# Optimization experiments

Hardware: AMD Instinct MI355X
Metric: run time of the kernel (lower is better)

The kernel has to match this reference:

```python
import jax, jax.numpy as jnp
import numpy as np

N_HEADS = 4
N_GROUPS = 32
EPS = 1e-5


def setup_inputs() -> dict:
    key = jax.random.key(0)
    ks = jax.random.split(key, 6)
    c = 512
    x = jax.random.normal(ks[0], (4, c, 64, 64), dtype=jnp.float32)
    # conv1x1 weights ~ kaiming-ish scale
    s = 1.0 / np.sqrt(c)
    wq = jax.random.normal(ks[1], (c, c), dtype=jnp.float32) * s
    wk = jax.random.normal(ks[2], (c, c), dtype=jnp.float32) * s
    wv = jax.random.normal(ks[3], (c, c), dtype=jnp.float32) * s
    wp = jax.random.normal(ks[4], (c, c), dtype=jnp.float32) * s
    zeros = jnp.zeros((c,), dtype=jnp.float32)
    return {
        "x": x,
        "gn_w": jnp.ones((c,), dtype=jnp.float32), "gn_b": zeros,
        "wq": wq, "bq": zeros, "wk": wk, "bk": zeros,
        "wv": wv, "bv": zeros, "wp": wp, "bp": zeros,
    }


def _group_norm(x, w, b):
    bsz, c, h, wd = x.shape
    xg = x.reshape(bsz, N_GROUPS, c // N_GROUPS, h, wd)
    mean = xg.mean(axis=(2, 3, 4), keepdims=True)
    var = xg.var(axis=(2, 3, 4), keepdims=True)
    xg = (xg - mean) * jax.lax.rsqrt(var + EPS)
    x = xg.reshape(bsz, c, h, wd)
    return x * w[None, :, None, None] + b[None, :, None, None]


def _conv1x1(x, w, b):
    # x: (b,c,h,w), w: (out,in) -> (b,out,h,w)
    return jnp.einsum('bchw,oc->bohw', x, w) + b[None, :, None, None]


def reference(x, gn_w, gn_b, wq, bq, wk, bk, wv, bv, wp, bp):
    bsz, c, h, wd = x.shape
    hd = c // N_HEADS
    hw = h * wd
    x_n = _group_norm(x, gn_w, gn_b)
    q = _conv1x1(x_n, wq, bq)
    k = _conv1x1(x_n, wk, bk)
    v = _conv1x1(x_n, wv, bv)

    def to_heads(t):
        # (b,c,h,w) -> (b, n_heads, hw, head_dim)
        return t.reshape(bsz, N_HEADS, hd, hw).transpose(0, 1, 3, 2)

    q, k, v = to_heads(q), to_heads(k), to_heads(v)
    scale = hd ** (-0.5)
    attn = jnp.einsum('bhqd,bhkd->bhqk', q, k) * scale  # (b,H,hw,hw)
    attn = jax.nn.softmax(attn, axis=-1)
    out = jnp.einsum('bhqk,bhkd->bhqd', attn, v)
    out = out.transpose(0, 1, 3, 2).reshape(bsz, c, h, wd)
    out = _conv1x1(out, wp, bp)
    return x + out
```

## Files before the change

### kernel.cpp

```cpp
#include <hip/hip_runtime.h>
#include <math.h>

typedef __attribute__((ext_vector_type(8))) short short8;
typedef __attribute__((ext_vector_type(4))) float floatx4;
typedef __attribute__((ext_vector_type(8))) unsigned short ushort8v;
typedef __attribute__((ext_vector_type(4))) unsigned short ushort4v;

#define HW 4096
#define CCH 512
#define NB 4
#define NH 4
#define HD 128

__device__ __forceinline__ unsigned short f2bf(float f) {
    union { float f; unsigned int u; } c; c.f = f;
    unsigned int u = c.u;
    u += 0x7FFFu + ((u >> 16) & 1u);
    return (unsigned short)(u >> 16);
}

__global__ void conv_w(const float* __restrict__ w0, const float* __restrict__ w1,
                       const float* __restrict__ w2, const float* __restrict__ w3,
                       unsigned short* __restrict__ dst) {
    const float* src = blockIdx.y == 0 ? w0 : blockIdx.y == 1 ? w1 : blockIdx.y == 2 ? w2 : w3;
    unsigned short* d = dst + (size_t)blockIdx.y * 262144;
    int i = blockIdx.x * 256 + threadIdx.x;
    float4 v = ((const float4*)src)[i];
    ushort4v o;
    o[0] = f2bf(v.x); o[1] = f2bf(v.y); o[2] = f2bf(v.z); o[3] = f2bf(v.w);
    ((ushort4v*)d)[i] = o;
}

__global__ void gn_stats(const float* __restrict__ x, float* __restrict__ stats) {
    int bg = blockIdx.x;
    int b = bg >> 5, g = bg & 31;
    const float4* p = (const float4*)(x + ((size_t)b * CCH + g * 16) * HW);
    float s = 0.f, ss = 0.f;
    for (int i = threadIdx.x; i < 16384; i += 256) {
        float4 v = p[i];
        s  += v.x + v.y + v.z + v.w;
        ss += v.x * v.x + v.y * v.y + v.z * v.z + v.w * v.w;
    }
    #pragma unroll
    for (int off = 32; off > 0; off >>= 1) {
        s  += __shfl_down(s, off, 64);
        ss += __shfl_down(ss, off, 64);
    }
    __shared__ float sm[4], sm2[4];
    int wid = threadIdx.x >> 6;
    if ((threadIdx.x & 63) == 0) { sm[wid] = s; sm2[wid] = ss; }
    __syncthreads();
    if (threadIdx.x == 0) {
        float ts = sm[0] + sm[1] + sm[2] + sm[3];
        float tss = sm2[0] + sm2[1] + sm2[2] + sm2[3];
        float mean = ts * (1.f / 65536.f);
        float var = tss * (1.f / 65536.f) - mean * mean;
        stats[bg * 2] = mean;
        stats[bg * 2 + 1] = rsqrtf(var + 1e-5f);
    }
}

__global__ void gn_apply(const float* __restrict__ x, const float* __restrict__ gnw,
                         const float* __restrict__ gnb, const float* __restrict__ stats,
                         unsigned short* __restrict__ xt) {
    int s = blockIdx.x * 256 + threadIdx.x;
    int g = blockIdx.y, b = blockIdx.z;
    float mean = stats[(b * 32 + g) * 2];
    float rstd = stats[(b * 32 + g) * 2 + 1];
    const float* xb = x + ((size_t)b * CCH + g * 16) * HW + s;
    unsigned short outv[16];
    #pragma unroll
    for (int cl = 0; cl < 16; cl++) {
        int c = g * 16 + cl;
        float v = xb[(size_t)cl * HW];
        v = (v - mean) * rstd * gnw[c] + gnb[c];
        outv[cl] = f2bf(v);
    }
    unsigned short* dst = xt + ((size_t)b * HW + s) * CCH + g * 16;
    *(ushort8v*)dst       = *(ushort8v*)&outv[0];
    *(ushort8v*)(dst + 8) = *(ushort8v*)&outv[8];
}

#define LDP 72
template <int MODE>
__global__ __launch_bounds__(256, 2) void gemm_nt(
    const unsigned short* __restrict__ A, long long aStride,
    const unsigned short* __restrict__ Bm, long long bStride,
    const float* __restrict__ bias, float scale,
    const float* __restrict__ resid, long long rStride,
    void* __restrict__ Cp, long long cStride, int ldc) {
    __shared__ unsigned short lA[128 * LDP];
    __shared__ unsigned short lB[128 * LDP];
    const int tid = threadIdx.x;
    const int lane = tid & 63;
    const int wid = tid >> 6;
    const int z = blockIdx.z;
    const unsigned short* Ab = A + (size_t)z * aStride + (size_t)blockIdx.x * 128 * 512;
    const unsigned short* Bb = Bm + (size_t)z * bStride + (size_t)blockIdx.y * 128 * 512;

    floatx4 acc[4][4];
    #pragma unroll
    for (int i = 0; i < 4; i++)
        #pragma unroll
        for (int j = 0; j < 4; j++) acc[i][j] = (floatx4)0.f;

    const int wm = (wid >> 1) * 64;
    const int wn = (wid & 1) * 64;
    const int l15 = lane & 15;
    const int l4 = lane >> 4;

    for (int k0 = 0; k0 < 512; k0 += 64) {
        #pragma unroll
        for (int i = 0; i < 4; i++) {
            int idx = i * 256 + tid;
            int row = idx >> 3;
            int kc = (idx & 7) * 8;
            *(ushort8v*)&lA[row * LDP + kc] = *(const ushort8v*)&Ab[(size_t)row * 512 + k0 + kc];
            *(ushort8v*)&lB[row * LDP + kc] = *(const ushort8v*)&Bb[(size_t)row * 512 + k0 + kc];
        }
        __syncthreads();
        #pragma unroll
        for (int kk = 0; kk < 2; kk++) {
            short8 af[4], bf[4];
            #pragma unroll
            for (int i = 0; i < 4; i++)
                af[i] = *(const short8*)&lA[(wm + i * 16 + l15) * LDP + kk * 32 + l4 * 8];
            #pragma unroll
            for (int j = 0; j < 4; j++)
                bf[j] = *(const short8*)&lB[(wn + j * 16 + l15) * LDP + kk * 32 + l4 * 8];
            #pragma unroll
            for (int i = 0; i < 4; i++)
                #pragma unroll
                for (int j = 0; j < 4; j++)
                    acc[i][j] = __builtin_amdgcn_mfma_f32_16x16x32_bf16(af[i], bf[j], acc[i][j], 0, 0, 0);
        }
        __syncthreads();
    }

    long long m0 = (long long)blockIdx.x * 128 + wm;
    long long n0 = (long long)blockIdx.y * 128 + wn;
    if (MODE == 0) {
        unsigned short* C = (unsigned short*)Cp + (size_t)z * cStride;
        #pragma unroll
        for (int i = 0; i < 4; i++)
            #pragma unroll
            for (int j = 0; j < 4; j++) {
                long long col = n0 + j * 16 + l15;
                float bv = bias[col];
                #pragma unroll
                for (int r = 0; r < 4; r++) {
                    long long row = m0 + i * 16 + l4 * 4 + r;
                    C[row * ldc + col] = f2bf((acc[i][j][r] + bv) * scale);
                }
            }
    } else if (MODE == 1) {
        float* C = (float*)Cp + (size_t)z * cStride;
        const float* R = resid + (size_t)z * rStride;
        #pragma unroll
        for (int i = 0; i < 4; i++)
            #pragma unroll
            for (int j = 0; j < 4; j++)
                #pragma unroll
                for (int r = 0; r < 4; r++) {
                    long long row = m0 + i * 16 + l4 * 4 + r;
                    long long col = n0 + j * 16 + l15;
                    C[row * ldc + col] = acc[i][j][r] + bias[row] + R[row * ldc + col];
                }
    } else {
        unsigned short* C = (unsigned short*)Cp + (size_t)z * cStride;
        #pragma unroll
        for (int i = 0; i < 4; i++)
            #pragma unroll
            for (int j = 0; j < 4; j++)
                #pragma unroll
                for (int r = 0; r < 4; r++) {
                    long long row = m0 + i * 16 + l4 * 4 + r;
                    long long col = n0 + j * 16 + l15;
                    C[row * ldc + col] = f2bf(acc[i][j][r] + bias[row]);
                }
    }
}

#define LQP 136
#define LTP 72
__global__ __launch_bounds__(256, 2) void attn_kern(
    const unsigned short* __restrict__ Qb, const unsigned short* __restrict__ Kb,
    const unsigned short* __restrict__ Vt, unsigned short* __restrict__ Ob) {
    __shared__ unsigned short lk[64 * LQP];
    __shared__ unsigned short lvt[128 * LTP];
    __shared__ unsigned short lp[128 * LTP];
    const int tid = threadIdx.x;
    const int lane = tid & 63;
    const int w = tid >> 6;
    const int l15 = lane & 15, l4 = lane >> 4;
    const int q0 = blockIdx.x * 128;
    const int h = blockIdx.y, b = blockIdx.z;
    const size_t headOff = (size_t)h * HD;
    const size_t batchRow = (size_t)b * HW;
    const unsigned short* VtB = Vt + ((size_t)b * CCH + headOff) * HW;

    short8 qf[2][4];
    #pragma unroll
    for (int i = 0; i < 2; i++)
        #pragma unroll
        for (int kk = 0; kk < 4; kk++)
            qf[i][kk] = *(const short8*)&Qb[(batchRow + q0 + w * 32 + i * 16 + l15) * 512
                                            + headOff + kk * 32 + l4 * 8];

    short8 onesf;
    {
        unsigned short o = (l15 == 0) ? (unsigned short)0x3F80 : (unsigned short)0;
        #pragma unroll
        for (int e = 0; e < 8; e++) onesf[e] = (short)o;
    }

    floatx4 acc_o[2][8];
    floatx4 acc_l[2];
    #pragma unroll
    for (int i = 0; i < 2; i++) {
        acc_l[i] = (floatx4)0.f;
        #pragma unroll
        for (int j = 0; j < 8; j++) acc_o[i][j] = (floatx4)0.f;
    }

    ushort8v kreg[4], vreg[4];
    #pragma unroll
    for (int i = 0; i < 4; i++) {
        int idx = i * 256 + tid;
        kreg[i] = *(const ushort8v*)&Kb[(batchRow + (idx >> 4)) * 512 + headOff + (idx & 15) * 8];
        vreg[i] = *(const ushort8v*)&VtB[(size_t)(idx >> 3) * HW + (idx & 7) * 8];
    }
    #pragma unroll
    for (int i = 0; i < 4; i++) {
        int idx = i * 256 + tid;
        *(ushort8v*)&lk[(idx >> 4) * LQP + (idx & 15) * 8] = kreg[i];
        *(ushort8v*)&lvt[(idx >> 3) * LTP + (idx & 7) * 8] = vreg[i];
    }
    __syncthreads();

    for (int kt = 0; kt < 64; kt++) {
        if (kt < 63) {
            int t0n = (kt + 1) * 64;
            #pragma unroll
            for (int i = 0; i < 4; i++) {
                int idx = i * 256 + tid;
                kreg[i] = *(const ushort8v*)&Kb[(batchRow + t0n + (idx >> 4)) * 512 + headOff + (idx & 15) * 8];
                vreg[i] = *(const ushort8v*)&VtB[(size_t)(idx >> 3) * HW + t0n + (idx & 7) * 8];
            }
        }

        floatx4 sa[2][4];
        #pragma unroll
        for (int i = 0; i < 2; i++)
            #pragma unroll
            for (int j = 0; j < 4; j++) sa[i][j] = (floatx4)0.f;
        #pragma unroll
        for (int kk = 0; kk < 4; kk++) {
            short8 bb[4];
            #pragma unroll
            for (int j = 0; j < 4; j++)
                bb[j] = *(const short8*)&lk[(j * 16 + l15) * LQP + kk * 32 + l4 * 8];
            #pragma unroll
            for (int i = 0; i < 2; i++)
                #pragma unroll
                for (int j = 0; j < 4; j++)
                    sa[i][j] = __builtin_amdgcn_mfma_f32_16x16x32_bf16(qf[i][kk], bb[j], sa[i][j], 0, 0, 0);
        }

        #pragma unroll
        for (int i = 0; i < 2; i++)
            #pragma unroll
            for (int j = 0; j < 4; j++)
                #pragma unroll
                for (int r = 0; r < 4; r++) {
                    float p = exp2f(sa[i][j][r]);
                    union { float f; unsigned int u; } c; c.f = p;
                    lp[(w * 32 + i * 16 + l4 * 4 + r) * LTP + j * 16 + l15] =
                        (unsigned short)((c.u + 0x8000u) >> 16);
                }

        #pragma unroll
        for (int ts = 0; ts < 2; ts++) {
            short8 pa[2];
            #pragma unroll
            for (int i = 0; i < 2; i++)
                pa[i] = *(const short8*)&lp[(w * 32 + i * 16 + l15) * LTP + ts * 32 + l4 * 8];
            #pragma unroll
            for (int j = 0; j < 8; j++) {
                short8 bb = *(const short8*)&lvt[(j * 16 + l15) * LTP + ts * 32 + l4 * 8];
                #pragma unroll
                for (int i = 0; i < 2; i++)
                    acc_o[i][j] = __builtin_amdgcn_mfma_f32_16x16x32_bf16(pa[i], bb, acc_o[i][j], 0, 0, 0);
            }
            #pragma unroll
            for (int i = 0; i < 2; i++)
                acc_l[i] = __builtin_amdgcn_mfma_f32_16x16x32_bf16(pa[i], onesf, acc_l[i], 0, 0, 0);
        }

        if (kt < 63) {
            __syncthreads();
            #pragma unroll
            for (int i = 0; i < 4; i++) {
                int idx = i * 256 + tid;
                *(ushort8v*)&lk[(idx >> 4) * LQP + (idx & 15) * 8] = kreg[i];
                *(ushort8v*)&lvt[(idx >> 3) * LTP + (idx & 7) * 8] = vreg[i];
            }
            __syncthreads();
        }
    }

    #pragma unroll
    for (int i = 0; i < 2; i++)
        #pragma unroll
        for (int r = 0; r < 4; r++) {
            float ls = __shfl(acc_l[i][r], lane & 48, 64);
            float rl = 1.f / ls;
            size_t row = batchRow + q0 + w * 32 + i * 16 + l4 * 4 + r;
            #pragma unroll
            for (int j = 0; j < 8; j++)
                Ob[row * 512 + headOff + j * 16 + l15] = f2bf(acc_o[i][j][r] * rl);
        }
}

extern "C" void kernel_launch(void* const* d_in, const int* in_sizes, int n_in,
                              void* d_out, int out_size, void* d_ws, size_t ws_size,
                              hipStream_t stream) {
    const float* x   = (const float*)d_in[0];
    const float* gnw = (const float*)d_in[1];
    const float* gnb = (const float*)d_in[2];
    const float* wq  = (const float*)d_in[3];
    const float* bq  = (const float*)d_in[4];
    const float* wk  = (const float*)d_in[5];
    const float* bk  = (const float*)d_in[6];
    const float* wv  = (const float*)d_in[7];
    const float* bv  = (const float*)d_in[8];
    const float* wp  = (const float*)d_in[9];
    const float* bp  = (const float*)d_in[10];
    float* out = (float*)d_out;

    const size_t NE = (size_t)NB * HW * CCH;
    unsigned short* ws16 = (unsigned short*)d_ws;
    unsigned short* XT = ws16;
    unsigned short* Qb = ws16 + NE;
    unsigned short* Kb = ws16 + 2 * NE;
    unsigned short* Vt = ws16 + 3 * NE;
    unsigned short* Wb = ws16 + 4 * NE;
    float* stats = (float*)(ws16 + 4 * NE + 4 * 262144);

    const float qscale = 0.08838834764831845f * 1.4426950408889634f;

    conv_w<<<dim3(256, 4), 256, 0, stream>>>(wq, wk, wv, wp, Wb);
    gn_stats<<<128, 256, 0, stream>>>(x, stats);
    gn_apply<<<dim3(16, 32, 4), 256, 0, stream>>>(x, gnw, gnb, stats, XT);

    gemm_nt<0><<<dim3(128, 4, 1), 256, 0, stream>>>(XT, 0, Wb + 0 * 262144, 0, bq, qscale, nullptr, 0, Qb, 0, 512);
    gemm_nt<0><<<dim3(128, 4, 1), 256, 0, stream>>>(XT, 0, Wb + 1 * 262144, 0, bk, 1.f, nullptr, 0, Kb, 0, 512);
    gemm_nt<2><<<dim3(4, 32, 4), 256, 0, stream>>>(Wb + 2 * 262144, 0, XT, (long long)HW * 512, bv, 1.f,
                                                   nullptr, 0, Vt, (long long)CCH * HW, HW);

    unsigned short* Ob = XT;
    attn_kern<<<dim3(32, NH, NB), 256, 0, stream>>>(Qb, Kb, Vt, Ob);

    gemm_nt<1><<<dim3(4, 32, 4), 256, 0, stream>>>(Wb + 3 * 262144, 0, Ob, (long long)HW * 512, bp, 1.f,
                                                   x, (long long)CCH * HW, out, (long long)CCH * HW, HW);
}
```

Before: 386.0 us.

## Double-buffer K/V tiles in attention via direct global-to-LDS DMA with swizzle

The attention kernel now loads K and V^T tiles straight into double-buffered LDS with global_load_lds instead of staging them through registers. It uses an XOR swizzle in place of padding to avoid bank conflicts and keeps one barrier per iteration instead of two. It also computes S transposed in 32-key half-tiles so the P buffer is smaller, and packs bf16 conversions in pairs with perm for the P and output stores. This removes register pressure and the copy from registers to LDS and overlaps loads with compute, at the cost of more LDS (two 32 KB stages) and more complex indexing that may limit occupancy.

```diff
diff --git a/kernel.cpp b/kernel.cpp
--- a/kernel.cpp
+++ b/kernel.cpp
@@ -5,6 +5,7 @@
 typedef __attribute__((ext_vector_type(4))) float floatx4;
 typedef __attribute__((ext_vector_type(8))) unsigned short ushort8v;
 typedef __attribute__((ext_vector_type(4))) unsigned short ushort4v;
+typedef __attribute__((ext_vector_type(2))) unsigned int uint2v;
 
 #define HW 4096
 #define CCH 512
@@ -17,6 +18,17 @@
     unsigned int u = c.u;
     u += 0x7FFFu + ((u >> 16) & 1u);
     return (unsigned short)(u >> 16);
+}
+
+__device__ __forceinline__ unsigned int pkbf(float a, float b) {
+    union { float f; unsigned int u; } x, y; x.f = a; y.f = b;
+    return __builtin_amdgcn_perm(y.u + 0x8000u, x.u + 0x8000u, 0x07060302u);
+}
+
+__device__ __forceinline__ void dma16(const unsigned short* g, unsigned short* l) {
+    __builtin_amdgcn_global_load_lds(
+        (const __attribute__((address_space(1))) unsigned int*)g,
+        (__attribute__((address_space(3))) unsigned int*)l, 16, 0, 0);
 }
 
 __global__ void conv_w(const float* __restrict__ w0, const float* __restrict__ w1,
@@ -181,18 +193,16 @@
     }
 }
 
-#define LQP 136
-#define LTP 72
+#define LPS 40
 __global__ __launch_bounds__(256, 2) void attn_kern(
     const unsigned short* __restrict__ Qb, const unsigned short* __restrict__ Kb,
     const unsigned short* __restrict__ Vt, unsigned short* __restrict__ Ob) {
-    __shared__ unsigned short lk[64 * LQP];
-    __shared__ unsigned short lvt[128 * LTP];
-    __shared__ unsigned short lp[128 * LTP];
+    __shared__ unsigned short stage[2][16384];
+    __shared__ unsigned short lp[128 * LPS];
     const int tid = threadIdx.x;
     const int lane = tid & 63;
     const int w = tid >> 6;
-    const int l15 = lane & 15, l4 = lane >> 4;
+    const int l15 = lane & 15, quad = lane >> 4;
     const int q0 = blockIdx.x * 128;
     const int h = blockIdx.y, b = blockIdx.z;
     const size_t headOff = (size_t)h * HD;
@@ -201,11 +211,11 @@
 
     short8 qf[2][4];
     #pragma unroll
-    for (int i = 0; i < 2; i++)
+    for (int n = 0; n < 2; n++)
         #pragma unroll
         for (int kk = 0; kk < 4; kk++)
-            qf[i][kk] = *(const short8*)&Qb[(batchRow + q0 + w * 32 + i * 16 + l15) * 512
-                                            + headOff + kk * 32 + l4 * 8];
+            qf[n][kk] = *(const short8*)&Qb[(batchRow + q0 + w * 32 + n * 16 + l15) * 512
+                                            + headOff + kk * 32 + quad * 8];
 
     short8 onesf;
     {
@@ -217,109 +227,126 @@
     floatx4 acc_o[2][8];
     floatx4 acc_l[2];
     #pragma unroll
-    for (int i = 0; i < 2; i++) {
-        acc_l[i] = (floatx4)0.f;
-        #pragma unroll
-        for (int j = 0; j < 8; j++) acc_o[i][j] = (floatx4)0.f;
-    }
-
-    ushort8v kreg[4], vreg[4];
-    #pragma unroll
-    for (int i = 0; i < 4; i++) {
-        int idx = i * 256 + tid;
-        kreg[i] = *(const ushort8v*)&Kb[(batchRow + (idx >> 4)) * 512 + headOff + (idx & 15) * 8];
-        vreg[i] = *(const ushort8v*)&VtB[(size_t)(idx >> 3) * HW + (idx & 7) * 8];
-    }
-    #pragma unroll
-    for (int i = 0; i < 4; i++) {
-        int idx = i * 256 + tid;
-        *(ushort8v*)&lk[(idx >> 4) * LQP + (idx & 15) * 8] = kreg[i];
-        *(ushort8v*)&lvt[(idx >> 3) * LTP + (idx & 7) * 8] = vreg[i];
-    }
+    for (int n = 0; n < 2; n++) {
+        acc_l[n] = (floatx4)0.f;
+        #pragma unroll
+        for (int i = 0; i < 8; i++) acc_o[n][i] = (floatx4)0.f;
+    }
+
+    const unsigned short* dmaPtr[8];
+    int dmaStep[8];
+    int ldsOff[8];
+    #pragma unroll
+    for (int t = 0; t < 8; t++) {
+        int R = w * 8192 + t * 1024;
+        ldsOff[t] = R;
+        if (R < 16384) {
+            int r = (R >> 8) + (lane >> 4);
+            int c = lane & 15;
+            int g = c ^ (r & 15);
+            dmaPtr[t] = Kb + (batchRow + r) * 512 + headOff + g * 8;
+            dmaStep[t] = 64 * 512;
+        } else {
+            int R2 = R - 16384;
+            int d = (R2 >> 7) + (lane >> 3);
+            int c = lane & 7;
+            int g = c ^ (d & 7);
+            dmaPtr[t] = VtB + (size_t)d * HW + g * 8;
+            dmaStep[t] = 64;
+        }
+    }
+
+    #pragma unroll
+    for (int t = 0; t < 8; t++)
+        dma16(dmaPtr[t], (unsigned short*)((char*)&stage[0][0] + ldsOff[t]));
     __syncthreads();
 
+    int p = 0;
     for (int kt = 0; kt < 64; kt++) {
         if (kt < 63) {
-            int t0n = (kt + 1) * 64;
-            #pragma unroll
-            for (int i = 0; i < 4; i++) {
-                int idx = i * 256 + tid;
-                kreg[i] = *(const ushort8v*)&Kb[(batchRow + t0n + (idx >> 4)) * 512 + headOff + (idx & 15) * 8];
-                vreg[i] = *(const ushort8v*)&VtB[(size_t)(idx >> 3) * HW + t0n + (idx & 7) * 8];
+            char* nb = (char*)&stage[p ^ 1][0];
+            #pragma unroll
+            for (int t = 0; t < 8; t++) {
+                dmaPtr[t] += dmaStep[t];
+                dma16(dmaPtr[t], (unsigned short*)(nb + ldsOff[t]));
             }
         }
-
-        floatx4 sa[2][4];
-        #pragma unroll
-        for (int i = 0; i < 2; i++)
-            #pragma unroll
-            for (int j = 0; j < 4; j++) sa[i][j] = (floatx4)0.f;
-        #pragma unroll
-        for (int kk = 0; kk < 4; kk++) {
-            short8 bb[4];
-            #pragma unroll
-            for (int j = 0; j < 4; j++)
-                bb[j] = *(const short8*)&lk[(j * 16 + l15) * LQP + kk * 32 + l4 * 8];
-            #pragma unroll
-            for (int i = 0; i < 2; i++)
-                #pragma unroll
-                for (int j = 0; j < 4; j++)
-                    sa[i][j] = __builtin_amdgcn_mfma_f32_16x16x32_bf16(qf[i][kk], bb[j], sa[i][j], 0, 0, 0);
-        }
-
-        #pragma unroll
-        for (int i = 0; i < 2; i++)
-            #pragma unroll
-            for (int j = 0; j < 4; j++)
-                #pragma unroll
-                for (int r = 0; r < 4; r++) {
-                    float p = exp2f(sa[i][j][r]);
-                    union { float f; unsigned int u; } c; c.f = p;
-                    lp[(w * 32 + i * 16 + l4 * 4 + r) * LTP + j * 16 + l15] =
-                        (unsigned short)((c.u + 0x8000u) >> 16);
-                }
+        const unsigned short* lk = &stage[p][0];
+        const unsigned short* lvt = &stage[p][8192];
 
         #pragma unroll
         for (int ts = 0; ts < 2; ts++) {
+            floatx4 sacc[2][2];
+            #pragma unroll
+            for (int mi = 0; mi < 2; mi++)
+                #pragma unroll
+                for (int n = 0; n < 2; n++) sacc[mi][n] = (floatx4)0.f;
+            #pragma unroll
+            for (int kk = 0; kk < 4; kk++) {
+                short8 ka[2];
+                #pragma unroll
+                for (int mi = 0; mi < 2; mi++) {
+                    int t = (ts * 2 + mi) * 16 + l15;
+                    int c = (kk * 4 + quad) ^ l15;
+                    ka[mi] = *(const short8*)&lk[t * 128 + c * 8];
+                }
+                #pragma unroll
+                for (int mi = 0; mi < 2; mi++)
+                    #pragma unroll
+                    for (int n = 0; n < 2; n++)
+                        sacc[mi][n] = __builtin_amdgcn_mfma_f32_16x16x32_bf16(ka[mi], qf[n][kk], sacc[mi][n], 0, 0, 0);
+            }
+
+            #pragma unroll
+            for (int mi = 0; mi < 2; mi++)
+                #pragma unroll
+                for (int n = 0; n < 2; n++) {
+                    float e0 = exp2f(sacc[mi][n][0]);
+                    float e1 = exp2f(sacc[mi][n][1]);
+                    float e2 = exp2f(sacc[mi][n][2]);
+                    float e3 = exp2f(sacc[mi][n][3]);
+                    uint2v pk;
+                    pk[0] = pkbf(e0, e1);
+                    pk[1] = pkbf(e2, e3);
+                    *(uint2v*)&lp[(w * 32 + n * 16 + l15) * LPS + mi * 16 + quad * 4] = pk;
+                }
+
             short8 pa[2];
             #pragma unroll
-            for (int i = 0; i < 2; i++)
-                pa[i] = *(const short8*)&lp[(w * 32 + i * 16 + l15) * LTP + ts * 32 + l4 * 8];
-            #pragma unroll
-            for (int j = 0; j < 8; j++) {
-                short8 bb = *(const short8*)&lvt[(j * 16 + l15) * LTP + ts * 32 + l4 * 8];
-                #pragma unroll
-                for (int i = 0; i < 2; i++)
-                    acc_o[i][j] = __builtin_amdgcn_mfma_f32_16x16x32_bf16(pa[i], bb, acc_o[i][j], 0, 0, 0);
+            for (int n = 0; n < 2; n++)
+                pa[n] = *(const short8*)&lp[(w * 32 + n * 16 + l15) * LPS + quad * 8];
+            #pragma unroll
+            for (int n = 0; n < 2; n++)
+                acc_l[n] = __builtin_amdgcn_mfma_f32_16x16x32_bf16(onesf, pa[n], acc_l[n], 0, 0, 0);
+            #pragma unroll
+            for (int i = 0; i < 8; i++) {
+                int d = i * 16 + l15;
+                int c = (ts * 4 + quad) ^ (l15 & 7);
+                short8 va = *(const short8*)&lvt[d * 64 + c * 8];
+                #pragma unroll
+                for (int n = 0; n < 2; n++)
+                    acc_o[n][i] = __builtin_amdgcn_mfma_f32_16x16x32_bf16(va, pa[n], acc_o[n][i], 0, 0, 0);
             }
-            #pragma unroll
-            for (int i = 0; i < 2; i++)
-                acc_l[i] = __builtin_amdgcn_mfma_f32_16x16x32_bf16(pa[i], onesf, acc_l[i], 0, 0, 0);
-        }
-
-        if (kt < 63) {
-            __syncthreads();
-            #pragma unroll
-            for (int i = 0; i < 4; i++) {
-                int idx = i * 256 + tid;
-                *(ushort8v*)&lk[(idx >> 4) * LQP + (idx & 15) * 8] = kreg[i];
-                *(ushort8v*)&lvt[(idx >> 3) * LTP + (idx & 7) * 8] = vreg[i];
-            }
-            __syncthreads();
-        }
-    }
-
-    #pragma unroll
-    for (int i = 0; i < 2; i++)
-        #pragma unroll
-        for (int r = 0; r < 4; r++) {
-            float ls = __shfl(acc_l[i][r], lane & 48, 64);
-            float rl = 1.f / ls;
-            size_t row = batchRow + q0 + w * 32 + i * 16 + l4 * 4 + r;
-            #pragma unroll
-            for (int j = 0; j < 8; j++)
-                Ob[row * 512 + headOff + j * 16 + l15] = f2bf(acc_o[i][j][r] * rl);
-        }
+        }
+
+        __syncthreads();
+        p ^= 1;
+    }
+
+    #pragma unroll
+    for (int n = 0; n < 2; n++) {
+        float ls = __shfl(acc_l[n][0], l15, 64);
+        float rl = 1.f / ls;
+        size_t srow = batchRow + q0 + w * 32 + n * 16 + l15;
+        unsigned short* obp = Ob + srow * 512 + headOff + quad * 4;
+        #pragma unroll
+        for (int i = 0; i < 8; i++) {
+            uint2v pk;
+            pk[0] = pkbf(acc_o[n][i][0] * rl, acc_o[n][i][1] * rl);
+            pk[1] = pkbf(acc_o[n][i][2] * rl, acc_o[n][i][3] * rl);
+            *(uint2v*)(obp + i * 16) = pk;
+        }
+    }
 }
 
 extern "C" void kernel_launch(void* const* d_in, const int* in_sizes, int n_in,
```

Result: no change. 387.0 us (+0.2%).
